# Kernel tuning notes

Measured on AMD Instinct MI355X. Metric: run time of the kernel, lower is better.

The kernel has to match this reference:

```python
import jax, jax.numpy as jnp
import numpy as np

DIM, DEPTH, MULT = 512, 3, 4
E = 2 ** DEPTH            # 8 experts
HID = MULT * DIM          # 2048
B, S = 4, 1024


def setup_inputs() -> dict:
    key = jax.random.key(0)
    ks = jax.random.split(key, 7)
    sd = 1.0 / np.sqrt(DIM)
    sh = 1.0 / np.sqrt(HID)
    return {
        "x": jax.random.normal(ks[0], (B, S, DIM), dtype=jnp.float32),
        "rw": jax.random.normal(ks[1], (E - 1, DIM), dtype=jnp.float32) * sd,
        "rb": jax.random.normal(ks[2], (E - 1,), dtype=jnp.float32) * sd,
        "w1": jax.random.normal(ks[3], (E, DIM, HID), dtype=jnp.float32) * sd,
        "b1": jax.random.normal(ks[4], (E, HID), dtype=jnp.float32) * sd,
        "w2": jax.random.normal(ks[5], (E, HID, DIM), dtype=jnp.float32) * sh,
        "b2": jax.random.normal(ks[6], (E, DIM), dtype=jnp.float32) * sh,
    }


def _leaf_probs(flat_x, rw, rb):
    # Binary-tree soft routing: level d has 2**d routers at offset 2**d - 1.
    n_tok = flat_x.shape[0]
    leaf = jnp.ones((n_tok, 1), dtype=flat_x.dtype)
    for d in range(DEPTH):
        off, n = 2 ** d - 1, 2 ** d
        logits = flat_x @ rw[off:off + n].T + rb[off:off + n]   # [N, n]
        p = jax.nn.sigmoid(logits)
        # child probs: left = 1-p, right = p
        leaf = (leaf[:, :, None] * jnp.stack([1.0 - p, p], axis=2)).reshape(n_tok, 2 * n)
    return leaf  # [N, E]


def reference(x, rw, rb, w1, b1, w2, b2):
    b, s, dim = x.shape
    flat_x = x.reshape(b * s, dim)                               # [N, D]
    leaf_probs = _leaf_probs(flat_x, rw, rb)                     # [N, E]
    # Dense evaluation of all experts (soft-routing training path).
    h = jnp.einsum('nd,edh->neh', flat_x, w1) + b1[None]         # [N, E, H]
    h = jax.nn.gelu(h, approximate=False)                        # torch nn.GELU (erf)
    y = jnp.einsum('neh,ehd->ned', h, w2) + b2[None]             # [N, E, D]
    out = jnp.einsum('ned,ne->nd', y, leaf_probs)                # [N, D]
    return out.reshape(b, s, dim)
```

## Files before the change

kernel.cpp:

```cpp
#include <hip/hip_runtime.h>
#include <hip/hip_bf16.h>
#include <hip/hip_fp16.h>

#define DIM 512
#define HID 2048
#define NE 8
#define NTOK 4096

typedef _Float16 v8h __attribute__((ext_vector_type(8)));
typedef float v16f __attribute__((ext_vector_type(16)));

__device__ __forceinline__ void load16(const void* g, void* l) {
  __builtin_amdgcn_global_load_lds(
      (const __attribute__((address_space(1))) unsigned int*)g,
      (__attribute__((address_space(3))) unsigned int*)l, 16, 0, 0);
}

__device__ __forceinline__ float gelu_fast(float v) {
  float v2 = v * v;
  float u = v * __builtin_fmaf(0.07135481627f, v2, 1.5957691216f);
  float t = __expf(-u);
  return v * __builtin_amdgcn_rcpf(1.0f + t);
}

__global__ __launch_bounds__(256) void pre_kernel(const float* __restrict__ x,
                                                  const float* __restrict__ rw,
                                                  const float* __restrict__ rb,
                                                  const float* __restrict__ b2,
                                                  const float* __restrict__ w1,
                                                  const float* __restrict__ w2,
                                                  float* __restrict__ leaf,
                                                  _Float16* __restrict__ xh,
                                                  float* __restrict__ out,
                                                  _Float16* __restrict__ w1t,
                                                  _Float16* __restrict__ w2t) {
  __shared__ float tile[32][65];
  if (blockIdx.x < 1024) {
    const int lane = threadIdx.x & 63;
    const int wave = threadIdx.x >> 6;
    const int n = (blockIdx.x << 2) + wave;
    const float4* xv = (const float4*)(x + (size_t)n * DIM);
    const float4 x0 = xv[lane * 2], x1 = xv[lane * 2 + 1];
    v8h o;
    o[0] = (_Float16)x0.x; o[1] = (_Float16)x0.y; o[2] = (_Float16)x0.z; o[3] = (_Float16)x0.w;
    o[4] = (_Float16)x1.x; o[5] = (_Float16)x1.y; o[6] = (_Float16)x1.z; o[7] = (_Float16)x1.w;
    *(v8h*)(xh + (size_t)n * DIM + lane * 8) = o;
    float logits[7];
#pragma unroll
    for (int rr = 0; rr < 7; ++rr) {
      const float4* wv = (const float4*)(rw + rr * DIM);
      const float4 w0 = wv[lane * 2], w1v = wv[lane * 2 + 1];
      float s = x0.x * w0.x + x0.y * w0.y + x0.z * w0.z + x0.w * w0.w +
                x1.x * w1v.x + x1.y * w1v.y + x1.z * w1v.z + x1.w * w1v.w;
#pragma unroll
      for (int o2 = 32; o2; o2 >>= 1) s += __shfl_xor(s, o2, 64);
      logits[rr] = s + rb[rr];
    }
    const int eidx = lane & 7;
    const float p0 = 1.f / (1.f + __expf(-logits[0]));
    float f = ((eidx >> 2) & 1) ? p0 : 1.f - p0;
    const float p1 = 1.f / (1.f + __expf(-logits[1 + (eidx >> 2)]));
    f *= ((eidx >> 1) & 1) ? p1 : 1.f - p1;
    const float p2 = 1.f / (1.f + __expf(-logits[3 + (eidx >> 1)]));
    f *= (eidx & 1) ? p2 : 1.f - p2;
    if (lane < NE) leaf[(size_t)n * NE + lane] = f;
    float le[NE];
#pragma unroll
    for (int e = 0; e < NE; ++e) le[e] = __shfl(f, e, 64);
    float4 a0 = {0.f, 0.f, 0.f, 0.f}, a1 = {0.f, 0.f, 0.f, 0.f};
#pragma unroll
    for (int e = 0; e < NE; ++e) {
      const float4* bv = (const float4*)(b2 + (size_t)e * DIM + lane * 8);
      const float4 u0 = bv[0], u1 = bv[1];
      a0.x += le[e] * u0.x; a0.y += le[e] * u0.y; a0.z += le[e] * u0.z; a0.w += le[e] * u0.w;
      a1.x += le[e] * u1.x; a1.y += le[e] * u1.y; a1.z += le[e] * u1.z; a1.w += le[e] * u1.w;
    }
    float4* op = (float4*)(out + (size_t)n * DIM + lane * 8);
    op[0] = a0; op[1] = a1;
  } else {
    int bx = blockIdx.x - 1024;
    const float* in;
    _Float16* outp;
    int R, C;
    if (bx < 4096) { in = w1; outp = w1t; R = DIM; C = HID; }
    else { bx -= 4096; in = w2; outp = w2t; R = HID; C = DIM; }
    const int e = bx >> 9;
    const int rem = bx & 511;
    const int tiles_r = R >> 6;
    const int rt = rem % tiles_r;
    const int ct = rem / tiles_r;
    const int r0 = rt << 6, c0 = ct << 5;
    const size_t ebase = (size_t)e * R * C;
    const int tid = threadIdx.x;
#pragma unroll
    for (int it = 0; it < 2; ++it) {
      const int s = tid + (it << 8);
      const int row = s >> 3, cq = s & 7;
      const float4 v = *(const float4*)(in + ebase + (size_t)(r0 + row) * C + c0 + (cq << 2));
      tile[(cq << 2) + 0][row] = v.x;
      tile[(cq << 2) + 1][row] = v.y;
      tile[(cq << 2) + 2][row] = v.z;
      tile[(cq << 2) + 3][row] = v.w;
    }
    __syncthreads();
    const int c = tid >> 3, seg = tid & 7;
    v8h hv;
#pragma unroll
    for (int u = 0; u < 8; ++u) hv[u] = (_Float16)tile[c][(seg << 3) + u];
    *(v8h*)(outp + ebase + (size_t)(c0 + c) * R + r0 + (seg << 3)) = hv;
  }
}

__global__ __launch_bounds__(256, 2) void gemm1_kernel(const _Float16* __restrict__ xh,
                                                       const _Float16* __restrict__ w1t,
                                                       const float* __restrict__ b1,
                                                       const float* __restrict__ leaf,
                                                       _Float16* __restrict__ H) {
  const int bx = blockIdx.x;
  const int e = bx & 7;
  const int t = bx >> 3;
  const int mt = t & 15;
  const int nt = t >> 4;
  const int m0 = mt << 8, n0 = nt << 7;

  __shared__ alignas(16) _Float16 As[256 * 64];
  __shared__ alignas(16) _Float16 Bs[128 * 64];

  const int tid = threadIdx.x;
  const int lane = tid & 63;
  const int wave = tid >> 6;
  const int wm = wave >> 1, wn = wave & 1;
  const int c = lane & 31, h2 = lane >> 5;
  const int cx = c & 7;

  const int strow = tid >> 3;
  const int c8 = (tid & 7) ^ (strow & 7);
  const _Float16* pa[8];
  const _Float16* pb[4];
  _Float16* la[8];
  _Float16* lb[4];
#pragma unroll
  for (int i = 0; i < 8; ++i) {
    pa[i] = xh + (size_t)(m0 + strow + 32 * i) * DIM + (c8 << 3);
    la[i] = As + tid * 8 + i * 2048;
  }
#pragma unroll
  for (int i = 0; i < 4; ++i) {
    pb[i] = w1t + ((size_t)e * HID + n0 + strow + 32 * i) * DIM + (c8 << 3);
    lb[i] = Bs + tid * 8 + i * 2048;
  }
  const _Float16* fA[4];
  const _Float16* fB[2];
#pragma unroll
  for (int i = 0; i < 4; ++i) fA[i] = As + ((wm << 7) + (i << 5) + c) * 64;
#pragma unroll
  for (int j = 0; j < 2; ++j) fB[j] = Bs + ((wn << 6) + (j << 5) + c) * 64;

  v16f acc[4][2];
#pragma unroll
  for (int i = 0; i < 4; ++i)
#pragma unroll
    for (int j = 0; j < 2; ++j)
      acc[i][j] = v16f{0.f,0.f,0.f,0.f,0.f,0.f,0.f,0.f,0.f,0.f,0.f,0.f,0.f,0.f,0.f,0.f};

#pragma unroll
  for (int kk = 0; kk < 8; ++kk) {
#pragma unroll
    for (int i = 0; i < 8; ++i) load16(pa[i] + kk * 64, la[i]);
#pragma unroll
    for (int i = 0; i < 4; ++i) load16(pb[i] + kk * 64, lb[i]);
    __syncthreads();
#pragma unroll
    for (int ks = 0; ks < 4; ++ks) {
      const int so = ((((ks << 1) + h2) ^ cx) << 3);
      v8h a[4], b[2];
#pragma unroll
      for (int i = 0; i < 4; ++i) a[i] = *(const v8h*)(fA[i] + so);
#pragma unroll
      for (int j = 0; j < 2; ++j) b[j] = *(const v8h*)(fB[j] + so);
#pragma unroll
      for (int i = 0; i < 4; ++i)
#pragma unroll
        for (int j = 0; j < 2; ++j)
          acc[i][j] = __builtin_amdgcn_mfma_f32_32x32x16_f16(a[i], b[j], acc[i][j], 0, 0, 0);
    }
    __syncthreads();
  }

  const float* b1e = b1 + (size_t)e * HID;
  _Float16* He = H + (size_t)e * NTOK * HID;
  const int colb = n0 + (wn << 6) + c;
  const float bias0 = b1e[colb];
  const float bias1 = b1e[colb + 32];
#pragma unroll
  for (int i = 0; i < 4; ++i) {
    const int rb0 = m0 + (wm << 7) + (i << 5) + (h2 << 2);
#pragma unroll
    for (int rg = 0; rg < 4; ++rg) {
#pragma unroll
      for (int rr = 0; rr < 4; ++rr) {
        const int row = rb0 + (rg << 3) + rr;
        const int reg = (rg << 2) + rr;
        const float p = leaf[(size_t)row * NE + e];
        _Float16* hp = He + (size_t)row * HID + colb;
        hp[0]  = (_Float16)(p * gelu_fast(acc[i][0][reg] + bias0));
        hp[32] = (_Float16)(p * gelu_fast(acc[i][1][reg] + bias1));
      }
    }
  }
}

__global__ __launch_bounds__(256, 2) void gemm2_kernel(const _Float16* __restrict__ H,
                                                       const _Float16* __restrict__ w2t,
                                                       float* __restrict__ out) {
  const int bx = blockIdx.x;
  const int e = bx & 7;
  const int dt = (bx >> 3) & 3;
  const int mt = bx >> 5;
  const int m0 = mt << 8, d0 = dt << 7;

  __shared__ alignas(16) _Float16 As[256 * 64];
  __shared__ alignas(16) _Float16 Bs[128 * 64];

  const int tid = threadIdx.x;
  const int lane = tid & 63;
  const int wave = tid >> 6;
  const int wm = wave >> 1, wn = wave & 1;
  const int c = lane & 31, h2 = lane >> 5;
  const int cx = c & 7;

  const int strow = tid >> 3;
  const int c8 = (tid & 7) ^ (strow & 7);
  const _Float16* pa[8];
  const _Float16* pb[4];
  _Float16* la[8];
  _Float16* lb[4];
#pragma unroll
  for (int i = 0; i < 8; ++i) {
    pa[i] = H + ((size_t)e * NTOK + m0 + strow + 32 * i) * HID + (c8 << 3);
    la[i] = As + tid * 8 + i * 2048;
  }
#pragma unroll
  for (int i = 0; i < 4; ++i) {
    pb[i] = w2t + ((size_t)e * DIM + d0 + strow + 32 * i) * HID + (c8 << 3);
    lb[i] = Bs + tid * 8 + i * 2048;
  }
  const _Float16* fA[4];
  const _Float16* fB[2];
#pragma unroll
  for (int i = 0; i < 4; ++i) fA[i] = As + ((wm << 7) + (i << 5) + c) * 64;
#pragma unroll
  for (int j = 0; j < 2; ++j) fB[j] = Bs + ((wn << 6) + (j << 5) + c) * 64;

  v16f acc[4][2];
#pragma unroll
  for (int i = 0; i < 4; ++i)
#pragma unroll
    for (int j = 0; j < 2; ++j)
      acc[i][j] = v16f{0.f,0.f,0.f,0.f,0.f,0.f,0.f,0.f,0.f,0.f,0.f,0.f,0.f,0.f,0.f,0.f};

  for (int ko = 0; ko < 4; ++ko) {
#pragma unroll
    for (int u = 0; u < 8; ++u) {
#pragma unroll
      for (int i = 0; i < 8; ++i) load16(pa[i] + u * 64, la[i]);
#pragma unroll
      for (int i = 0; i < 4; ++i) load16(pb[i] + u * 64, lb[i]);
      __syncthreads();
#pragma unroll
      for (int ks = 0; ks < 4; ++ks) {
        const int so = ((((ks << 1) + h2) ^ cx) << 3);
        v8h a[4], b[2];
#pragma unroll
        for (int i = 0; i < 4; ++i) a[i] = *(const v8h*)(fA[i] + so);
#pragma unroll
        for (int j = 0; j < 2; ++j) b[j] = *(const v8h*)(fB[j] + so);
#pragma unroll
        for (int i = 0; i < 4; ++i)
#pragma unroll
          for (int j = 0; j < 2; ++j)
            acc[i][j] = __builtin_amdgcn_mfma_f32_32x32x16_f16(a[i], b[j], acc[i][j], 0, 0, 0);
      }
      __syncthreads();
    }
#pragma unroll
    for (int i = 0; i < 8; ++i) pa[i] += 512;
#pragma unroll
    for (int i = 0; i < 4; ++i) pb[i] += 512;
  }

#pragma unroll
  for (int i = 0; i < 4; ++i) {
    const int rb0 = m0 + (wm << 7) + (i << 5) + (h2 << 2);
#pragma unroll
    for (int rg = 0; rg < 4; ++rg) {
#pragma unroll
      for (int rr = 0; rr < 4; ++rr) {
        const int row = rb0 + (rg << 3) + rr;
        const int reg = (rg << 2) + rr;
        float* op = out + (size_t)row * DIM + d0 + (wn << 6) + c;
        atomicAdd(op, acc[i][0][reg]);
        atomicAdd(op + 32, acc[i][1][reg]);
      }
    }
  }
}

extern "C" void kernel_launch(void* const* d_in, const int* in_sizes, int n_in,
                              void* d_out, int out_size, void* d_ws, size_t ws_size,
                              hipStream_t stream) {
  const float* x  = (const float*)d_in[0];
  const float* rw = (const float*)d_in[1];
  const float* rb = (const float*)d_in[2];
  const float* w1 = (const float*)d_in[3];
  const float* b1 = (const float*)d_in[4];
  const float* w2 = (const float*)d_in[5];
  const float* b2 = (const float*)d_in[6];
  float* out = (float*)d_out;

  char* ws = (char*)d_ws;
  const size_t xh_bytes   = (size_t)NTOK * DIM * 2;
  const size_t w1t_bytes  = (size_t)NE * HID * DIM * 2;
  const size_t w2t_bytes  = (size_t)NE * DIM * HID * 2;
  const size_t leaf_bytes = (size_t)NTOK * NE * 4;
  const size_t H_bytes    = (size_t)NE * NTOK * HID * 2;
  _Float16* xh   = (_Float16*)(ws);
  _Float16* w1t  = (_Float16*)(ws + xh_bytes);
  _Float16* w2t  = (_Float16*)(ws + xh_bytes + w1t_bytes);
  float*    leaf = (float*)(ws + xh_bytes + w1t_bytes + w2t_bytes);
  _Float16* Hbuf = (_Float16*)(ws + xh_bytes + w1t_bytes + w2t_bytes + leaf_bytes);
  if (ws_size < xh_bytes + w1t_bytes + w2t_bytes + leaf_bytes + H_bytes) return;

  pre_kernel<<<9216, 256, 0, stream>>>(x, rw, rb, b2, w1, w2, leaf, xh, out, w1t, w2t);
  gemm1_kernel<<<2048, 256, 0, stream>>>(xh, w1t, b1, leaf, Hbuf);
  gemm2_kernel<<<512, 256, 0, stream>>>(Hbuf, w2t, out);
}
```

Before: 328.5 us.

## Double-buffer LDS tiles with K=32 stages to overlap loads and MFMA

Both expert GEMM kernels switch from a single 64-wide K tile, loaded then computed with a barrier between, to two 32-wide K buffers in LDS. The next stage's global-to-LDS loads are issued before the current stage's MFMAs run, and the LDS XOR swizzle is redone for the 32-element row width. The goal is to hide global load latency behind matrix math while keeping the same total LDS footprint. In exchange there are more barriers per K element and a narrower swizzle that could raise bank conflicts.

Result: slower. 347.4 us (+5.7%).

```diff
diff --git a/kernel.cpp b/kernel.cpp
--- a/kernel.cpp
+++ b/kernel.cpp
@@ -111,6 +111,34 @@
   }
 }
 
+
+#define GEMM_STAGE(AO_LDS, BO_LDS, KOFF)                                      \
+  {                                                                           \
+    _Pragma("unroll") for (int p = 0; p < 4; ++p)                             \
+        load16(ga[p] + (KOFF), la[p] + (AO_LDS));                             \
+    _Pragma("unroll") for (int p = 0; p < 2; ++p)                             \
+        load16(gb[p] + (KOFF), lb[p] + (BO_LDS));                             \
+  }
+
+#define GEMM_COMPUTE(AO, BO)                                                  \
+  {                                                                           \
+    v8h a[4], b[2];                                                           \
+    _Pragma("unroll") for (int i = 0; i < 4; ++i)                             \
+        a[i] = *(const v8h*)(fA[i] + (AO) + po0);                             \
+    _Pragma("unroll") for (int j = 0; j < 2; ++j)                             \
+        b[j] = *(const v8h*)(fB[j] + (BO) + po0);                             \
+    _Pragma("unroll") for (int i = 0; i < 4; ++i)                             \
+        _Pragma("unroll") for (int j = 0; j < 2; ++j)                         \
+            acc[i][j] = __builtin_amdgcn_mfma_f32_32x32x16_f16(a[i], b[j], acc[i][j], 0, 0, 0); \
+    _Pragma("unroll") for (int i = 0; i < 4; ++i)                             \
+        a[i] = *(const v8h*)(fA[i] + (AO) + (po0 ^ 16));                      \
+    _Pragma("unroll") for (int j = 0; j < 2; ++j)                             \
+        b[j] = *(const v8h*)(fB[j] + (BO) + (po0 ^ 16));                      \
+    _Pragma("unroll") for (int i = 0; i < 4; ++i)                             \
+        _Pragma("unroll") for (int j = 0; j < 2; ++j)                         \
+            acc[i][j] = __builtin_amdgcn_mfma_f32_32x32x16_f16(a[i], b[j], acc[i][j], 0, 0, 0); \
+  }
+
 __global__ __launch_bounds__(256, 2) void gemm1_kernel(const _Float16* __restrict__ xh,
                                                        const _Float16* __restrict__ w1t,
                                                        const float* __restrict__ b1,
@@ -123,38 +151,43 @@
   const int nt = t >> 4;
   const int m0 = mt << 8, n0 = nt << 7;
 
-  __shared__ alignas(16) _Float16 As[256 * 64];
-  __shared__ alignas(16) _Float16 Bs[128 * 64];
+  __shared__ alignas(16) _Float16 As[2 * 256 * 32];
+  __shared__ alignas(16) _Float16 Bs[2 * 128 * 32];
 
   const int tid = threadIdx.x;
   const int lane = tid & 63;
   const int wave = tid >> 6;
   const int wm = wave >> 1, wn = wave & 1;
   const int c = lane & 31, h2 = lane >> 5;
-  const int cx = c & 7;
-
-  const int strow = tid >> 3;
-  const int c8 = (tid & 7) ^ (strow & 7);
-  const _Float16* pa[8];
-  const _Float16* pb[4];
-  _Float16* la[8];
-  _Float16* lb[4];
-#pragma unroll
-  for (int i = 0; i < 8; ++i) {
-    pa[i] = xh + (size_t)(m0 + strow + 32 * i) * DIM + (c8 << 3);
-    la[i] = As + tid * 8 + i * 2048;
-  }
-#pragma unroll
-  for (int i = 0; i < 4; ++i) {
-    pb[i] = w1t + ((size_t)e * HID + n0 + strow + 32 * i) * DIM + (c8 << 3);
-    lb[i] = Bs + tid * 8 + i * 2048;
+  const int swz = (c >> 1) & 3;
+  const int po0 = (h2 ^ swz) << 3;
+
+  const _Float16* ga[4];
+  const _Float16* gb[2];
+  _Float16* la[4];
+  _Float16* lb[2];
+#pragma unroll
+  for (int p = 0; p < 4; ++p) {
+    const int ci = (p << 8) + tid;
+    const int row = ci >> 2;
+    const int lg = (ci & 3) ^ ((row >> 1) & 3);
+    ga[p] = xh + (size_t)(m0 + row) * DIM + (lg << 3);
+    la[p] = As + (ci << 3);
+  }
+#pragma unroll
+  for (int p = 0; p < 2; ++p) {
+    const int ci = (p << 8) + tid;
+    const int row = ci >> 2;
+    const int lg = (ci & 3) ^ ((row >> 1) & 3);
+    gb[p] = w1t + ((size_t)e * HID + n0 + row) * DIM + (lg << 3);
+    lb[p] = Bs + (ci << 3);
   }
   const _Float16* fA[4];
   const _Float16* fB[2];
 #pragma unroll
-  for (int i = 0; i < 4; ++i) fA[i] = As + ((wm << 7) + (i << 5) + c) * 64;
-#pragma unroll
-  for (int j = 0; j < 2; ++j) fB[j] = Bs + ((wn << 6) + (j << 5) + c) * 64;
+  for (int i = 0; i < 4; ++i) fA[i] = As + (((wm << 7) + (i << 5) + c) << 5);
+#pragma unroll
+  for (int j = 0; j < 2; ++j) fB[j] = Bs + (((wn << 6) + (j << 5) + c) << 5);
 
   v16f acc[4][2];
 #pragma unroll
@@ -163,29 +196,24 @@
     for (int j = 0; j < 2; ++j)
       acc[i][j] = v16f{0.f,0.f,0.f,0.f,0.f,0.f,0.f,0.f,0.f,0.f,0.f,0.f,0.f,0.f,0.f,0.f};
 
-#pragma unroll
-  for (int kk = 0; kk < 8; ++kk) {
-#pragma unroll
-    for (int i = 0; i < 8; ++i) load16(pa[i] + kk * 64, la[i]);
-#pragma unroll
-    for (int i = 0; i < 4; ++i) load16(pb[i] + kk * 64, lb[i]);
-    __syncthreads();
-#pragma unroll
-    for (int ks = 0; ks < 4; ++ks) {
-      const int so = ((((ks << 1) + h2) ^ cx) << 3);
-      v8h a[4], b[2];
-#pragma unroll
-      for (int i = 0; i < 4; ++i) a[i] = *(const v8h*)(fA[i] + so);
-#pragma unroll
-      for (int j = 0; j < 2; ++j) b[j] = *(const v8h*)(fB[j] + so);
-#pragma unroll
-      for (int i = 0; i < 4; ++i)
-#pragma unroll
-        for (int j = 0; j < 2; ++j)
-          acc[i][j] = __builtin_amdgcn_mfma_f32_32x32x16_f16(a[i], b[j], acc[i][j], 0, 0, 0);
-    }
-    __syncthreads();
-  }
+  GEMM_STAGE(0, 0, 0);
+  __syncthreads();
+  for (int gp = 0; gp < 7; ++gp) {
+    GEMM_STAGE(8192, 4096, 32);
+    GEMM_COMPUTE(0, 0);
+    __syncthreads();
+    GEMM_STAGE(0, 0, 64);
+    GEMM_COMPUTE(8192, 4096);
+    __syncthreads();
+#pragma unroll
+    for (int p = 0; p < 4; ++p) ga[p] += 64;
+#pragma unroll
+    for (int p = 0; p < 2; ++p) gb[p] += 64;
+  }
+  GEMM_STAGE(8192, 4096, 32);
+  GEMM_COMPUTE(0, 0);
+  __syncthreads();
+  GEMM_COMPUTE(8192, 4096);
 
   const float* b1e = b1 + (size_t)e * HID;
   _Float16* He = H + (size_t)e * NTOK * HID;
@@ -219,38 +247,43 @@
   const int mt = bx >> 5;
   const int m0 = mt << 8, d0 = dt << 7;
 
-  __shared__ alignas(16) _Float16 As[256 * 64];
-  __shared__ alignas(16) _Float16 Bs[128 * 64];
+  __shared__ alignas(16) _Float16 As[2 * 256 * 32];
+  __shared__ alignas(16) _Float16 Bs[2 * 128 * 32];
 
   const int tid = threadIdx.x;
   const int lane = tid & 63;
   const int wave = tid >> 6;
   const int wm = wave >> 1, wn = wave & 1;
   const int c = lane & 31, h2 = lane >> 5;
-  const int cx = c & 7;
-
-  const int strow = tid >> 3;
-  const int c8 = (tid & 7) ^ (strow & 7);
-  const _Float16* pa[8];
-  const _Float16* pb[4];
-  _Float16* la[8];
-  _Float16* lb[4];
-#pragma unroll
-  for (int i = 0; i < 8; ++i) {
-    pa[i] = H + ((size_t)e * NTOK + m0 + strow + 32 * i) * HID + (c8 << 3);
-    la[i] = As + tid * 8 + i * 2048;
-  }
-#pragma unroll
-  for (int i = 0; i < 4; ++i) {
-    pb[i] = w2t + ((size_t)e * DIM + d0 + strow + 32 * i) * HID + (c8 << 3);
-    lb[i] = Bs + tid * 8 + i * 2048;
+  const int swz = (c >> 1) & 3;
+  const int po0 = (h2 ^ swz) << 3;
+
+  const _Float16* ga[4];
+  const _Float16* gb[2];
+  _Float16* la[4];
+  _Float16* lb[2];
+#pragma unroll
+  for (int p = 0; p < 4; ++p) {
+    const int ci = (p << 8) + tid;
+    const int row = ci >> 2;
+    const int lg = (ci & 3) ^ ((row >> 1) & 3);
+    ga[p] = H + ((size_t)e * NTOK + m0 + row) * HID + (lg << 3);
+    la[p] = As + (ci << 3);
+  }
+#pragma unroll
+  for (int p = 0; p < 2; ++p) {
+    const int ci = (p << 8) + tid;
+    const int row = ci >> 2;
+    const int lg = (ci & 3) ^ ((row >> 1) & 3);
+    gb[p] = w2t + ((size_t)e * DIM + d0 + row) * HID + (lg << 3);
+    lb[p] = Bs + (ci << 3);
   }
   const _Float16* fA[4];
   const _Float16* fB[2];
 #pragma unroll
-  for (int i = 0; i < 4; ++i) fA[i] = As + ((wm << 7) + (i << 5) + c) * 64;
-#pragma unroll
-  for (int j = 0; j < 2; ++j) fB[j] = Bs + ((wn << 6) + (j << 5) + c) * 64;
+  for (int i = 0; i < 4; ++i) fA[i] = As + (((wm << 7) + (i << 5) + c) << 5);
+#pragma unroll
+  for (int j = 0; j < 2; ++j) fB[j] = Bs + (((wn << 6) + (j << 5) + c) << 5);
 
   v16f acc[4][2];
 #pragma unroll
@@ -259,35 +292,24 @@
     for (int j = 0; j < 2; ++j)
       acc[i][j] = v16f{0.f,0.f,0.f,0.f,0.f,0.f,0.f,0.f,0.f,0.f,0.f,0.f,0.f,0.f,0.f,0.f};
 
-  for (int ko = 0; ko < 4; ++ko) {
-#pragma unroll
-    for (int u = 0; u < 8; ++u) {
-#pragma unroll
-      for (int i = 0; i < 8; ++i) load16(pa[i] + u * 64, la[i]);
-#pragma unroll
-      for (int i = 0; i < 4; ++i) load16(pb[i] + u * 64, lb[i]);
-      __syncthreads();
-#pragma unroll
-      for (int ks = 0; ks < 4; ++ks) {
-        const int so = ((((ks << 1) + h2) ^ cx) << 3);
-        v8h a[4], b[2];
-#pragma unroll
-        for (int i = 0; i < 4; ++i) a[i] = *(const v8h*)(fA[i] + so);
-#pragma unroll
-        for (int j = 0; j < 2; ++j) b[j] = *(const v8h*)(fB[j] + so);
-#pragma unroll
-        for (int i = 0; i < 4; ++i)
-#pragma unroll
-          for (int j = 0; j < 2; ++j)
-            acc[i][j] = __builtin_amdgcn_mfma_f32_32x32x16_f16(a[i], b[j], acc[i][j], 0, 0, 0);
-      }
-      __syncthreads();
-    }
-#pragma unroll
-    for (int i = 0; i < 8; ++i) pa[i] += 512;
-#pragma unroll
-    for (int i = 0; i < 4; ++i) pb[i] += 512;
-  }
+  GEMM_STAGE(0, 0, 0);
+  __syncthreads();
+  for (int gp = 0; gp < 31; ++gp) {
+    GEMM_STAGE(8192, 4096, 32);
+    GEMM_COMPUTE(0, 0);
+    __syncthreads();
+    GEMM_STAGE(0, 0, 64);
+    GEMM_COMPUTE(8192, 4096);
+    __syncthreads();
+#pragma unroll
+    for (int p = 0; p < 4; ++p) ga[p] += 64;
+#pragma unroll
+    for (int p = 0; p < 2; ++p) gb[p] += 64;
+  }
+  GEMM_STAGE(8192, 4096, 32);
+  GEMM_COMPUTE(0, 0);
+  __syncthreads();
+  GEMM_COMPUTE(8192, 4096);
 
 #pragma unroll
   for (int i = 0; i < 4; ++i) {
```

## Split gemm2 along K, rewrite weight transpose without LDS, raise occupancy hint

Applied to the files above, without the earlier changes.

The weight transpose/convert in pre_kernel drops the shared-memory tile: each thread now reads 32 strided rows of one column and writes four contiguous fp16 vectors, with far fewer blocks. gemm2 is split into two K halves, doubling its grid to 1024 blocks so the single-wave tail on the GPU is less of a problem. Both GEMMs get a launch_bounds occupancy hint of 3. Risks: the strided column reads may coalesce worse, the occupancy hint may force register spills, and the K split only works if the (unseen) epilogue accumulates into out atomically.

After: 698.4 us. 113% more time.

```diff
diff --git a/kernel.cpp b/kernel.cpp
--- a/kernel.cpp
+++ b/kernel.cpp
@@ -34,7 +34,6 @@
                                                   float* __restrict__ out,
                                                   _Float16* __restrict__ w1t,
                                                   _Float16* __restrict__ w2t) {
-  __shared__ float tile[32][65];
   if (blockIdx.x < 1024) {
     const int lane = threadIdx.x & 63;
     const int wave = threadIdx.x >> 6;
@@ -78,40 +77,33 @@
     float4* op = (float4*)(out + (size_t)n * DIM + lane * 8);
     op[0] = a0; op[1] = a1;
   } else {
-    int bx = blockIdx.x - 1024;
+    int t = blockIdx.x - 1024;
     const float* in;
     _Float16* outp;
-    int R, C;
-    if (bx < 4096) { in = w1; outp = w1t; R = DIM; C = HID; }
-    else { bx -= 4096; in = w2; outp = w2t; R = HID; C = DIM; }
-    const int e = bx >> 9;
-    const int rem = bx & 511;
-    const int tiles_r = R >> 6;
-    const int rt = rem % tiles_r;
-    const int ct = rem / tiles_r;
-    const int r0 = rt << 6, c0 = ct << 5;
-    const size_t ebase = (size_t)e * R * C;
-    const int tid = threadIdx.x;
-#pragma unroll
-    for (int it = 0; it < 2; ++it) {
-      const int s = tid + (it << 8);
-      const int row = s >> 3, cq = s & 7;
-      const float4 v = *(const float4*)(in + ebase + (size_t)(r0 + row) * C + c0 + (cq << 2));
-      tile[(cq << 2) + 0][row] = v.x;
-      tile[(cq << 2) + 1][row] = v.y;
-      tile[(cq << 2) + 2][row] = v.z;
-      tile[(cq << 2) + 3][row] = v.w;
-    }
-    __syncthreads();
-    const int c = tid >> 3, seg = tid & 7;
-    v8h hv;
-#pragma unroll
-    for (int u = 0; u < 8; ++u) hv[u] = (_Float16)tile[c][(seg << 3) + u];
-    *(v8h*)(outp + ebase + (size_t)(c0 + c) * R + r0 + (seg << 3)) = hv;
-  }
-}
-
-__global__ __launch_bounds__(256, 2) void gemm1_kernel(const _Float16* __restrict__ xh,
+    int C, K, kb;
+    if (t < 1024) { in = w1; outp = w1t; C = HID; K = DIM; kb = 16; }
+    else { t -= 1024; in = w2; outp = w2t; C = DIM; K = HID; kb = 64; }
+    const int e = t >> 7;
+    const int rem = t & 127;
+    const int kt = rem % kb;
+    const int ntile = rem / kb;
+    const int k0 = kt << 5;
+    const int n = (ntile << 8) + threadIdx.x;
+    const size_t ebase = (size_t)e * K * C;
+    const float* src = in + ebase + (size_t)k0 * C + n;
+    v8h o[4];
+#pragma unroll
+    for (int g = 0; g < 4; ++g)
+#pragma unroll
+      for (int u = 0; u < 8; ++u)
+        o[g][u] = (_Float16)src[(size_t)(g * 8 + u) * C];
+    v8h* dst = (v8h*)(outp + ebase + (size_t)n * K + k0);
+#pragma unroll
+    for (int g = 0; g < 4; ++g) dst[g] = o[g];
+  }
+}
+
+__global__ __launch_bounds__(256, 3) void gemm1_kernel(const _Float16* __restrict__ xh,
                                                        const _Float16* __restrict__ w1t,
                                                        const float* __restrict__ b1,
                                                        const float* __restrict__ leaf,
@@ -210,14 +202,16 @@
   }
 }
 
-__global__ __launch_bounds__(256, 2) void gemm2_kernel(const _Float16* __restrict__ H,
+__global__ __launch_bounds__(256, 3) void gemm2_kernel(const _Float16* __restrict__ H,
                                                        const _Float16* __restrict__ w2t,
                                                        float* __restrict__ out) {
   const int bx = blockIdx.x;
   const int e = bx & 7;
   const int dt = (bx >> 3) & 3;
-  const int mt = bx >> 5;
+  const int mt = (bx >> 5) & 15;
+  const int kh = bx >> 9;
   const int m0 = mt << 8, d0 = dt << 7;
+  const int ka0 = kh << 10;
 
   __shared__ alignas(16) _Float16 As[256 * 64];
   __shared__ alignas(16) _Float16 Bs[128 * 64];
@@ -237,12 +231,12 @@
   _Float16* lb[4];
 #pragma unroll
   for (int i = 0; i < 8; ++i) {
-    pa[i] = H + ((size_t)e * NTOK + m0 + strow + 32 * i) * HID + (c8 << 3);
+    pa[i] = H + ((size_t)e * NTOK + m0 + strow + 32 * i) * HID + ka0 + (c8 << 3);
     la[i] = As + tid * 8 + i * 2048;
   }
 #pragma unroll
   for (int i = 0; i < 4; ++i) {
-    pb[i] = w2t + ((size_t)e * DIM + d0 + strow + 32 * i) * HID + (c8 << 3);
+    pb[i] = w2t + ((size_t)e * DIM + d0 + strow + 32 * i) * HID + ka0 + (c8 << 3);
     lb[i] = Bs + tid * 8 + i * 2048;
   }
   const _Float16* fA[4];
@@ -259,7 +253,7 @@
     for (int j = 0; j < 2; ++j)
       acc[i][j] = v16f{0.f,0.f,0.f,0.f,0.f,0.f,0.f,0.f,0.f,0.f,0.f,0.f,0.f,0.f,0.f,0.f};
 
-  for (int ko = 0; ko < 4; ++ko) {
+  for (int ko = 0; ko < 2; ++ko) {
 #pragma unroll
     for (int u = 0; u < 8; ++u) {
 #pragma unroll
@@ -331,7 +325,7 @@
   _Float16* Hbuf = (_Float16*)(ws + xh_bytes + w1t_bytes + w2t_bytes + leaf_bytes);
   if (ws_size < xh_bytes + w1t_bytes + w2t_bytes + leaf_bytes + H_bytes) return;
 
-  pre_kernel<<<9216, 256, 0, stream>>>(x, rw, rb, b2, w1, w2, leaf, xh, out, w1t, w2t);
+  pre_kernel<<<3072, 256, 0, stream>>>(x, rw, rb, b2, w1, w2, leaf, xh, out, w1t, w2t);
   gemm1_kernel<<<2048, 256, 0, stream>>>(xh, w1t, b1, leaf, Hbuf);
-  gemm2_kernel<<<512, 256, 0, stream>>>(Hbuf, w2t, out);
-}
+  gemm2_kernel<<<1024, 256, 0, stream>>>(Hbuf, w2t, out);
+}
```
